# Kernel optimization log

Measured on AMD Instinct MI355X. Metric: run time of the kernel, lower is better.

The kernel has to match this reference:

```python
import jax, jax.numpy as jnp
import numpy as np


def setup_inputs() -> dict:
    key = jax.random.key(0)
    k0, k1, k2, k3, k4 = jax.random.split(key, 5)
    B, H, W, C = 8, 64, 64, 256
    d = C // 8
    scale = 0.02
    return {
        "inputs": jax.random.normal(k0, (B, H, W, C), dtype=jnp.float32),
        "w_q": jax.random.normal(k1, (C, d), dtype=jnp.float32) * scale,
        "w_k": jax.random.normal(k2, (C, d), dtype=jnp.float32) * scale,
        "w_v": jax.random.normal(k3, (C, C), dtype=jnp.float32) * scale,
        "w_out": jax.random.normal(k4, (C, C), dtype=jnp.float32) * scale,
    }


def reference(inputs, w_q, w_k, w_v, w_out):
    B, H, W, C = inputs.shape
    N = H * W
    x = inputs.reshape(B, N, C)  # 1x1 conv == per-pixel channel matmul
    q = jnp.einsum("bnc,cd->bnd", x, w_q)   # [B, N, C//8]
    k = jnp.einsum("bnc,cd->bnd", x, w_k)   # [B, N, C//8]
    v = jnp.einsum("bnc,ce->bne", x, w_v)   # [B, N, C]
    attn = jax.nn.softmax(jnp.einsum("bnd,bmd->bnm", q, k), axis=-1)  # [B, N, N]
    attended = jnp.einsum("bnm,bme->bne", attn, v)  # [B, N, C]
    out = jnp.einsum("bne,ec->bnc", attended, w_out)
    return inputs + out.reshape(B, H, W, C)
```

## Files before the change

kernel.cpp:

```cpp
#include <hip/hip_runtime.h>
#include <hip/hip_bf16.h>
#include <stdint.h>

typedef __attribute__((ext_vector_type(8))) short short8;
typedef __attribute__((ext_vector_type(8))) unsigned short ushort8;
typedef __attribute__((ext_vector_type(4))) unsigned short ushort4v;
typedef __attribute__((ext_vector_type(4))) unsigned u32x4;
typedef __attribute__((ext_vector_type(2))) float f32x2;
typedef __attribute__((ext_vector_type(4))) float f32x4;
typedef __attribute__((ext_vector_type(16))) float f32x16;

#define B_ 8
#define N_ 4096
#define C_ 256
#define D_ 32
#define LOG2E 1.44269504088896f

__device__ inline unsigned short f2bf(float f) {
  union { float f; unsigned u; } v; v.f = f;
  unsigned r = v.u + 0x7fffu + ((v.u >> 16) & 1u);
  return (unsigned short)(r >> 16);
}
__device__ inline float bf2f(unsigned short u) {
  return __uint_as_float(((unsigned)u) << 16);
}
__device__ inline float exp2_fast(float x) {
  float r; asm("v_exp_f32 %0, %1" : "=v"(r) : "v"(x)); return r;
}
__device__ inline unsigned cvt_pk_bf16(float lo, float hi) {
  unsigned r; asm("v_cvt_pk_bf16_f32 %0, %1, %2" : "=v"(r) : "v"(lo), "v"(hi)); return r;
}
__device__ inline void permlane32_swap(unsigned& a, unsigned& b) {
  asm volatile("v_permlane32_swap_b32 %0, %1" : "+v"(a), "+v"(b));
}
__device__ inline void gll16(const unsigned short* src, void* lds) {
  __builtin_amdgcn_global_load_lds((const __attribute__((address_space(1))) void*)src,
                                   (__attribute__((address_space(3))) void*)lds, 16, 0, 0);
}

__device__ inline size_t wf_addr(int C, int kk) {
  int ct = C >> 4, cl = C & 15, s = kk >> 5, gf = (kk >> 3) & 3, j = kk & 7;
  return ((size_t)((ct * 8 + s) * 64 + gf * 16 + cl)) * 8 + j;
}

__global__ __launch_bounds__(256) void prep_kernel(const float* __restrict__ wq,
                                                   const float* __restrict__ wk,
                                                   const float* __restrict__ wo,
                                                   const float* __restrict__ wv,
                                                   unsigned short* __restrict__ wf,
                                                   unsigned short* __restrict__ wv_b,
                                                   unsigned short* __restrict__ woT_b) {
  int i = blockIdx.x * 256 + threadIdx.x;
  if (i < 16384) {
    int C = i >> 8, kk = i & 255;
    float v = (C < 32) ? wq[kk * 32 + C] * LOG2E : wk[kk * 32 + (C - 32)];
    wf[wf_addr(C, kk)] = f2bf(v);
  } else if (i < 81920) {
    int j = i - 16384;
    wv_b[j] = f2bf(wv[j]);
  } else {
    int j = i - 81920;
    int e2 = j >> 8, e = j & 255;
    woT_b[j] = f2bf(wo[e * 256 + e2]);
  }
}

__global__ __launch_bounds__(256) void prep2_kernel(const unsigned short* __restrict__ woT_b,
                                                    const unsigned short* __restrict__ wv_b,
                                                    unsigned short* __restrict__ wf) {
  const int lane = threadIdx.x & 63, w = threadIdx.x >> 6;
  const int g = lane >> 4, li = lane & 15;
  const int m0 = blockIdx.x * 64 + w * 16;
  const unsigned short* arow = woT_b + (size_t)(m0 + li) * 256 + (g << 3);
  const unsigned short* brow = wv_b + (size_t)li * 256 + (g << 3);
  f32x4 acc[16] = {};
  for (int kk = 0; kk < 256; kk += 32) {
    short8 a = *reinterpret_cast<const short8*>(arow + kk);
#pragma unroll
    for (int ct = 0; ct < 16; ++ct) {
      short8 bb = *reinterpret_cast<const short8*>(brow + (size_t)ct * 16 * 256 + kk);
      acc[ct] = __builtin_amdgcn_mfma_f32_16x16x32_bf16(a, bb, acc[ct], 0, 0, 0);
    }
  }
#pragma unroll
  for (int ct = 0; ct < 16; ++ct)
#pragma unroll
    for (int r = 0; r < 4; ++r) {
      const int C = 64 + m0 + (g << 2) + r;
      const int kk = ct * 16 + li;
      wf[wf_addr(C, kk)] = f2bf(acc[ct][r]);
    }
}

__global__ __launch_bounds__(256, 2) void qkv_kernel(const float* __restrict__ x,
                                                     const unsigned short* __restrict__ wf,
                                                     unsigned short* __restrict__ q,
                                                     unsigned short* __restrict__ k,
                                                     unsigned short* __restrict__ vwT) {
  __shared__ __align__(16) unsigned short xs[64 * 256];
  const int tid = threadIdx.x;
  const int l = tid & 63, w = tid >> 6;
  const int bx = blockIdx.x;
  const int g = l >> 4, li = l & 15;
  const int m0 = bx * 64;

  const unsigned short* wfb = wf + (size_t)(w * 5) * 4096;

  short8 BA[5], BB[5];
#pragma unroll
  for (int c = 0; c < 5; ++c)
    BA[c] = *reinterpret_cast<const short8*>(wfb + ((size_t)(c * 8 + 0) * 64 + l) * 8);
#pragma unroll
  for (int c = 0; c < 5; ++c)
    BB[c] = *reinterpret_cast<const short8*>(wfb + ((size_t)(c * 8 + 1) * 64 + l) * 8);

  {
    const int row = tid >> 2, qtr = tid & 3;
    const float* src = x + (size_t)(m0 + row) * 256 + qtr * 64;
    unsigned short* dstrow = xs + row * 256;
#pragma unroll
    for (int jj = 0; jj < 8; ++jj) {
      f32x4 a0 = *reinterpret_cast<const f32x4*>(src + jj * 8);
      f32x4 a1 = *reinterpret_cast<const f32x4*>(src + jj * 8 + 4);
      union { unsigned u[4]; ushort8 v; } P;
      P.u[0] = cvt_pk_bf16(a0[0], a0[1]); P.u[1] = cvt_pk_bf16(a0[2], a0[3]);
      P.u[2] = cvt_pk_bf16(a1[0], a1[1]); P.u[3] = cvt_pk_bf16(a1[2], a1[3]);
      const int blk = (qtr * 8 + jj) ^ (row & 7);
      *reinterpret_cast<ushort8*>(dstrow + blk * 8) = P.v;
    }
  }
  __syncthreads();

  f32x4 acc[4][5] = {};

#define QSTEP(S, BV, WN, PREF)                                                       \
  {                                                                                  \
    asm volatile("s_waitcnt vmcnt(" WN ")" ::: "memory");                            \
    __builtin_amdgcn_sched_barrier(0);                                               \
    short8 a_[4];                                                                    \
    _Pragma("unroll") for (int mt = 0; mt < 4; ++mt) {                               \
      const int row = mt * 16 + li;                                                  \
      a_[mt] = *reinterpret_cast<const short8*>(                                     \
          xs + row * 256 + ((((S) * 4 + g) ^ (row & 7)) << 3));                      \
    }                                                                                \
    _Pragma("unroll") for (int mt = 0; mt < 4; ++mt)                                 \
        _Pragma("unroll") for (int c = 0; c < 5; ++c)                                \
            acc[mt][c] = __builtin_amdgcn_mfma_f32_16x16x32_bf16(a_[mt], BV[c],      \
                                                                 acc[mt][c], 0, 0, 0); \
    if (PREF) {                                                                      \
      _Pragma("unroll") for (int c = 0; c < 5; ++c)                                  \
          BV[c] = *reinterpret_cast<const short8*>(                                  \
              wfb + ((size_t)(c * 8 + (S) + 2) * 64 + l) * 8);                       \
    }                                                                                \
  }

  QSTEP(0, BA, "5", true)
  QSTEP(1, BB, "5", true)
  QSTEP(2, BA, "5", true)
  QSTEP(3, BB, "5", true)
  QSTEP(4, BA, "5", true)
  QSTEP(5, BB, "5", true)
  QSTEP(6, BA, "5", false)
  QSTEP(7, BB, "0", false)
#undef QSTEP

  const int bb_ = bx >> 6;
#pragma unroll
  for (int mt = 0; mt < 4; ++mt) {
    const int nloc = (bx & 63) * 64 + mt * 16 + (g << 2);
#pragma unroll
    for (int c = 0; c < 5; ++c) {
      const int Cg = w * 5 + c;
      if (Cg < 2) {
        const int col = Cg * 16 + li;
#pragma unroll
        for (int r = 0; r < 4; ++r)
          q[((size_t)bb_ * N_ + nloc + r) * D_ + col] = f2bf(acc[mt][c][r]);
      } else if (Cg < 4) {
        const int col = (Cg - 2) * 16 + li;
#pragma unroll
        for (int r = 0; r < 4; ++r)
          k[((size_t)bb_ * N_ + nloc + r) * D_ + col] = f2bf(acc[mt][c][r]);
      } else {
        const int vc = Cg * 16 + li - 64;
        union { unsigned u[2]; ushort4v v; } P;
        P.u[0] = cvt_pk_bf16(acc[mt][c][0], acc[mt][c][1]);
        P.u[1] = cvt_pk_bf16(acc[mt][c][2], acc[mt][c][3]);
        *reinterpret_cast<ushort4v*>(&vwT[((size_t)bb_ * C_ + vc) * N_ + nloc]) = P.v;
      }
    }
  }
}

__global__ __launch_bounds__(512, 2) void flash_kernel(const unsigned short* __restrict__ q,
                                                       const unsigned short* __restrict__ k,
                                                       const unsigned short* __restrict__ vwT,
                                                       const float* __restrict__ x,
                                                       float* __restrict__ out) {
  __shared__ __align__(16) char smem[106496];
  const int tid = threadIdx.x;
  const int l = tid & 63, w_ = tid >> 6;
  const int kvh = w_ >> 2, gw = w_ & 3;
  const int qg = gw >> 1, ch = gw & 1;
  const int blk = blockIdx.x;
  const int b = blk & 7;
  const int qt = blk >> 3;
  const int h = l >> 5, l31 = l & 31;
  const int R = kvh * 53248;

  const unsigned short* kb_ = k + (size_t)b * N_ * D_;
  const unsigned short* vb_ = vwT + (size_t)b * C_ * N_;

  const int qposb = qt * 128 + qg * 64;
  short8 qb[2][2];
#pragma unroll
  for (int qt2 = 0; qt2 < 2; ++qt2) {
    const size_t qoff = ((size_t)b * N_ + qposb + qt2 * 32 + l31) * D_ + h * 8;
    qb[qt2][0] = *reinterpret_cast<const short8*>(q + qoff);
    qb[qt2][1] = *reinterpret_cast<const short8*>(q + qoff + 16);
  }
  asm volatile("s_waitcnt vmcnt(0)" ::: "memory");

  const int stg_row = l >> 2;
  const int stg_bk = ((l & 3) ^ ((l >> 3) & 3)) << 3;
  const int kvbase = kvh * 2048;

#define STAGE_V(BUF, KV0)                                                         \
  {                                                                               \
    char* vd = smem + R + (BUF) * 16384 + gw * 4096;                              \
    _Pragma("unroll") for (int t = 0; t < 4; ++t)                                 \
        gll16(vb_ + (size_t)(gw * 64 + t * 16 + stg_row) * N_ + (KV0) + stg_bk,   \
              vd + t * 1024);                                                     \
  }
#define STAGE_K(BUF, KV0)                                                         \
  {                                                                               \
    if (gw < 2)                                                                   \
      gll16(kb_ + (size_t)((KV0) + gw * 16 + stg_row) * D_ + stg_bk,              \
            smem + R + 49152 + (BUF) * 2048 + gw * 1024);                         \
  }

  f32x16 o[4][2] = {};
  float lsum[2] = {0.f, 0.f};
  const f32x16 z16 = {};

  STAGE_V(0, kvbase)
  STAGE_K(0, kvbase)
  STAGE_V(1, kvbase + 32)

  int cur = 0, nxt = 2;
  for (int i = 0; i < 64; ++i) {
    if (i < 63) { asm volatile("s_waitcnt vmcnt(4)" ::: "memory"); }
    else        { asm volatile("s_waitcnt vmcnt(0)" ::: "memory"); }
    __builtin_amdgcn_sched_barrier(0);
    __builtin_amdgcn_s_barrier();
    if (i < 63) STAGE_K((i + 1) & 1, kvbase + (i + 1) * 32)
    if (i < 62) STAGE_V(nxt, kvbase + (i + 2) * 32)
    const char* Vb = smem + R + cur * 16384;
    const char* Kb = smem + R + 49152 + (i & 1) * 2048;
    const int kkey = (l31 >> 1) & 3;
    short8 ka0 = *reinterpret_cast<const short8*>(Kb + l31 * 64 + (((0 + h) ^ kkey) << 4));
    short8 ka1 = *reinterpret_cast<const short8*>(Kb + l31 * 64 + (((2 + h) ^ kkey) << 4));
    f32x16 s0 = __builtin_amdgcn_mfma_f32_32x32x16_bf16(ka0, qb[0][0], z16, 0, 0, 0);
    s0 = __builtin_amdgcn_mfma_f32_32x32x16_bf16(ka1, qb[0][1], s0, 0, 0, 0);
    f32x16 s1 = __builtin_amdgcn_mfma_f32_32x32x16_bf16(ka0, qb[1][0], z16, 0, 0, 0);
    s1 = __builtin_amdgcn_mfma_f32_32x32x16_bf16(ka1, qb[1][1], s1, 0, 0, 0);
    short8 pf[2][2];
#pragma unroll
    for (int r = 0; r < 16; ++r) s0[r] = exp2_fast(s0[r]);
    if (ch == 0)
      lsum[0] += (((s0[0] + s0[1]) + (s0[2] + s0[3])) + ((s0[4] + s0[5]) + (s0[6] + s0[7]))) +
                 (((s0[8] + s0[9]) + (s0[10] + s0[11])) + ((s0[12] + s0[13]) + (s0[14] + s0[15])));
    {
      unsigned x0 = cvt_pk_bf16(s0[0], s0[1]),   y0 = cvt_pk_bf16(s0[4], s0[5]);
      unsigned x1 = cvt_pk_bf16(s0[2], s0[3]),   y1 = cvt_pk_bf16(s0[6], s0[7]);
      unsigned x2 = cvt_pk_bf16(s0[8], s0[9]),   y2 = cvt_pk_bf16(s0[12], s0[13]);
      unsigned x3 = cvt_pk_bf16(s0[10], s0[11]), y3 = cvt_pk_bf16(s0[14], s0[15]);
      permlane32_swap(x0, y0); permlane32_swap(x1, y1);
      permlane32_swap(x2, y2); permlane32_swap(x3, y3);
      union U { unsigned u[4]; short8 v; };
      U u0; u0.u[0] = x0; u0.u[1] = x1; u0.u[2] = y0; u0.u[3] = y1;
      U u1; u1.u[0] = x2; u1.u[1] = x3; u1.u[2] = y2; u1.u[3] = y3;
      pf[0][0] = u0.v; pf[0][1] = u1.v;
    }
#pragma unroll
    for (int r = 0; r < 16; ++r) s1[r] = exp2_fast(s1[r]);
    if (ch == 0)
      lsum[1] += (((s1[0] + s1[1]) + (s1[2] + s1[3])) + ((s1[4] + s1[5]) + (s1[6] + s1[7]))) +
                 (((s1[8] + s1[9]) + (s1[10] + s1[11])) + ((s1[12] + s1[13]) + (s1[14] + s1[15])));
    {
      unsigned x0 = cvt_pk_bf16(s1[0], s1[1]),   y0 = cvt_pk_bf16(s1[4], s1[5]);
      unsigned x1 = cvt_pk_bf16(s1[2], s1[3]),   y1 = cvt_pk_bf16(s1[6], s1[7]);
      unsigned x2 = cvt_pk_bf16(s1[8], s1[9]),   y2 = cvt_pk_bf16(s1[12], s1[13]);
      unsigned x3 = cvt_pk_bf16(s1[10], s1[11]), y3 = cvt_pk_bf16(s1[14], s1[15]);
      permlane32_swap(x0, y0); permlane32_swap(x1, y1);
      permlane32_swap(x2, y2); permlane32_swap(x3, y3);
      union U { unsigned u[4]; short8 v; };
      U u0; u0.u[0] = x0; u0.u[1] = x1; u0.u[2] = y0; u0.u[3] = y1;
      U u1; u1.u[0] = x2; u1.u[1] = x3; u1.u[2] = y2; u1.u[3] = y3;
      pf[1][0] = u0.v; pf[1][1] = u1.v;
    }
    __builtin_amdgcn_s_setprio(1);
#pragma unroll
    for (int ct = 0; ct < 4; ++ct) {
      const int rl = ch * 128 + ct * 32 + l31;
      const int vkey = (rl >> 1) & 3;
      short8 va0 = *reinterpret_cast<const short8*>(Vb + rl * 64 + (((0 + h) ^ vkey) << 4));
      short8 va1 = *reinterpret_cast<const short8*>(Vb + rl * 64 + (((2 + h) ^ vkey) << 4));
      o[ct][0] = __builtin_amdgcn_mfma_f32_32x32x16_bf16(va0, pf[0][0], o[ct][0], 0, 0, 0);
      o[ct][0] = __builtin_amdgcn_mfma_f32_32x32x16_bf16(va1, pf[0][1], o[ct][0], 0, 0, 0);
      o[ct][1] = __builtin_amdgcn_mfma_f32_32x32x16_bf16(va0, pf[1][0], o[ct][1], 0, 0, 0);
      o[ct][1] = __builtin_amdgcn_mfma_f32_32x32x16_bf16(va1, pf[1][1], o[ct][1], 0, 0, 0);
    }
    __builtin_amdgcn_s_setprio(0);
    cur = (cur == 2) ? 0 : cur + 1;
    nxt = (nxt == 2) ? 0 : nxt + 1;
  }

  lsum[0] += __shfl_xor(lsum[0], 32);
  lsum[1] += __shfl_xor(lsum[1], 32);
  __syncthreads();
  float* lb = reinterpret_cast<float*>(smem + 65536);
  if (ch == 0 && h == 0) {
    lb[kvh * 128 + qg * 64 + l31] = lsum[0];
    lb[kvh * 128 + qg * 64 + 32 + l31] = lsum[1];
  }
  if (kvh == 1) {
    char* ob = smem + gw * 16384;
    int pg = 0;
#pragma unroll
    for (int ct = 0; ct < 4; ++ct)
#pragma unroll
      for (int qt2 = 0; qt2 < 2; ++qt2)
#pragma unroll
        for (int jg = 0; jg < 2; ++jg) {
          u32x4 t;
#pragma unroll
          for (int e = 0; e < 4; ++e) {
            const int j = jg * 4 + e;
            t[e] = cvt_pk_bf16(o[ct][qt2][2 * j], o[ct][qt2][2 * j + 1]);
          }
          *reinterpret_cast<u32x4*>(ob + pg * 1024 + l * 16) = t;
          ++pg;
        }
  }
  __syncthreads();
  if (kvh == 0) {
    float inv[2];
#pragma unroll
    for (int qt2 = 0; qt2 < 2; ++qt2)
      inv[qt2] = 1.0f / (lb[qg * 64 + qt2 * 32 + l31] + lb[128 + qg * 64 + qt2 * 32 + l31]);
    const char* ob = smem + gw * 16384;
    int pg = 0;
#pragma unroll
    for (int ct = 0; ct < 4; ++ct)
#pragma unroll
      for (int qt2 = 0; qt2 < 2; ++qt2)
#pragma unroll
        for (int jg = 0; jg < 2; ++jg) {
          u32x4 t = *reinterpret_cast<const u32x4*>(ob + pg * 1024 + l * 16);
          ++pg;
#pragma unroll
          for (int e = 0; e < 4; ++e) {
            const int j = jg * 4 + e;
            o[ct][qt2][2 * j]     += bf2f((unsigned short)(t[e] & 0xffffu));
            o[ct][qt2][2 * j + 1] += bf2f((unsigned short)(t[e] >> 16));
          }
        }
#pragma unroll
    for (int qt2 = 0; qt2 < 2; ++qt2) {
      const size_t rowbase = ((size_t)b * N_ + qposb + qt2 * 32 + l31) * C_ + ch * 128;
#pragma unroll
      for (int ct = 0; ct < 4; ++ct)
#pragma unroll
        for (int j = 0; j < 8; ++j) {
          const int c = ct * 32 + 2 * (j & 1) + 8 * (j >> 1) + 4 * h;
          f32x2 xr = *reinterpret_cast<const f32x2*>(x + rowbase + c);
          f32x2 t;
          t[0] = o[ct][qt2][2 * j] * inv[qt2] + xr[0];
          t[1] = o[ct][qt2][2 * j + 1] * inv[qt2] + xr[1];
          *reinterpret_cast<f32x2*>(out + rowbase + c) = t;
        }
    }
  }
#undef STAGE_V
#undef STAGE_K
}

extern "C" void kernel_launch(void* const* d_in, const int* in_sizes, int n_in,
                              void* d_out, int out_size, void* d_ws, size_t ws_size,
                              hipStream_t stream) {
  const float* x  = (const float*)d_in[0];
  const float* wq = (const float*)d_in[1];
  const float* wk = (const float*)d_in[2];
  const float* wv = (const float*)d_in[3];
  const float* wo = (const float*)d_in[4];
  float* out = (float*)d_out;
  char* ws = (char*)d_ws;
  unsigned short* wf    = (unsigned short*)(ws + 0);
  unsigned short* wv_b  = (unsigned short*)(ws + 163840);
  unsigned short* woT_b = (unsigned short*)(ws + 294912);
  unsigned short* q     = (unsigned short*)(ws + 425984);
  unsigned short* k     = (unsigned short*)(ws + 2523136);
  unsigned short* vwT   = (unsigned short*)(ws + 4620288);

  prep_kernel<<<576, 256, 0, stream>>>(wq, wk, wo, wv, wf, wv_b, woT_b);
  prep2_kernel<<<4, 256, 0, stream>>>(woT_b, wv_b, wf);
  qkv_kernel<<<512, 256, 0, stream>>>(x, wf, q, k, vwT);
  flash_kernel<<<256, 512, 0, stream>>>(q, k, vwT, x, out);
}
```

Measured before the change: 139.5 us.

## Double KV tile to 64 with double-buffered LDS staging of K and V

Each loop iteration now processes 64 keys instead of 32, so the flash loop runs 32 iterations with half as many block barriers. The old triple-buffered V ring with separate K staging becomes a single double-buffered stage that loads K and V together, using an 8-way XOR swizzle on the wider V rows. The aim is to amortise barrier and wait overhead over more MFMA work per iteration. In exchange LDS grows to 144KB and the wait is now a full vmcnt(0), so prefetch runs only one tile ahead and hides less latency.

```diff
diff --git a/kernel.cpp b/kernel.cpp
--- a/kernel.cpp
+++ b/kernel.cpp
@@ -197,7 +197,7 @@
                                                        const unsigned short* __restrict__ vwT,
                                                        const float* __restrict__ x,
                                                        float* __restrict__ out) {
-  __shared__ __align__(16) char smem[106496];
+  __shared__ __align__(16) char smem[147456];
   const int tid = threadIdx.x;
   const int l = tid & 63, w_ = tid >> 6;
   const int kvh = w_ >> 2, gw = w_ & 3;
@@ -206,7 +206,7 @@
   const int b = blk & 7;
   const int qt = blk >> 3;
   const int h = l >> 5, l31 = l & 31;
-  const int R = kvh * 53248;
+  const int R = kvh * 65536;
 
   const unsigned short* kb_ = k + (size_t)b * N_ * D_;
   const unsigned short* vb_ = vwT + (size_t)b * C_ * N_;
@@ -221,105 +221,102 @@
   }
   asm volatile("s_waitcnt vmcnt(0)" ::: "memory");
 
-  const int stg_row = l >> 2;
-  const int stg_bk = ((l & 3) ^ ((l >> 3) & 3)) << 3;
+  const int vrow = l >> 3;
+  const int vsrc = ((l & 7) ^ ((l >> 3) & 7)) << 3;
+  const int krow = l >> 2;
+  const int ksrc = ((l & 3) ^ ((l >> 3) & 3)) << 3;
   const int kvbase = kvh * 2048;
 
-#define STAGE_V(BUF, KV0)                                                         \
+#define STAGE(BUF, KV0)                                                           \
   {                                                                               \
-    char* vd = smem + R + (BUF) * 16384 + gw * 4096;                              \
-    _Pragma("unroll") for (int t = 0; t < 4; ++t)                                 \
-        gll16(vb_ + (size_t)(gw * 64 + t * 16 + stg_row) * N_ + (KV0) + stg_bk,   \
+    char* vd = smem + R + (BUF) * 32768 + gw * 8192;                              \
+    _Pragma("unroll") for (int t = 0; t < 8; ++t)                                 \
+        gll16(vb_ + (size_t)(gw * 64 + t * 8 + vrow) * N_ + (KV0) + vsrc,         \
               vd + t * 1024);                                                     \
-  }
-#define STAGE_K(BUF, KV0)                                                         \
-  {                                                                               \
-    if (gw < 2)                                                                   \
-      gll16(kb_ + (size_t)((KV0) + gw * 16 + stg_row) * D_ + stg_bk,              \
-            smem + R + 49152 + (BUF) * 2048 + gw * 1024);                         \
+    gll16(kb_ + (size_t)((KV0) + gw * 16 + krow) * D_ + ksrc,                     \
+          smem + 131072 + kvh * 8192 + (BUF) * 4096 + gw * 1024);                 \
   }
 
   f32x16 o[4][2] = {};
   float lsum[2] = {0.f, 0.f};
   const f32x16 z16 = {};
-
-  STAGE_V(0, kvbase)
-  STAGE_K(0, kvbase)
-  STAGE_V(1, kvbase + 32)
-
-  int cur = 0, nxt = 2;
-  for (int i = 0; i < 64; ++i) {
-    if (i < 63) { asm volatile("s_waitcnt vmcnt(4)" ::: "memory"); }
-    else        { asm volatile("s_waitcnt vmcnt(0)" ::: "memory"); }
+  const int kkey = (l31 >> 1) & 3;
+
+  STAGE(0, kvbase)
+
+  for (int i = 0; i < 32; ++i) {
+    const int buf = i & 1;
+    asm volatile("s_waitcnt vmcnt(0)" ::: "memory");
     __builtin_amdgcn_sched_barrier(0);
     __builtin_amdgcn_s_barrier();
-    if (i < 63) STAGE_K((i + 1) & 1, kvbase + (i + 1) * 32)
-    if (i < 62) STAGE_V(nxt, kvbase + (i + 2) * 32)
-    const char* Vb = smem + R + cur * 16384;
-    const char* Kb = smem + R + 49152 + (i & 1) * 2048;
-    const int kkey = (l31 >> 1) & 3;
-    short8 ka0 = *reinterpret_cast<const short8*>(Kb + l31 * 64 + (((0 + h) ^ kkey) << 4));
-    short8 ka1 = *reinterpret_cast<const short8*>(Kb + l31 * 64 + (((2 + h) ^ kkey) << 4));
-    f32x16 s0 = __builtin_amdgcn_mfma_f32_32x32x16_bf16(ka0, qb[0][0], z16, 0, 0, 0);
-    s0 = __builtin_amdgcn_mfma_f32_32x32x16_bf16(ka1, qb[0][1], s0, 0, 0, 0);
-    f32x16 s1 = __builtin_amdgcn_mfma_f32_32x32x16_bf16(ka0, qb[1][0], z16, 0, 0, 0);
-    s1 = __builtin_amdgcn_mfma_f32_32x32x16_bf16(ka1, qb[1][1], s1, 0, 0, 0);
-    short8 pf[2][2];
-#pragma unroll
-    for (int r = 0; r < 16; ++r) s0[r] = exp2_fast(s0[r]);
-    if (ch == 0)
-      lsum[0] += (((s0[0] + s0[1]) + (s0[2] + s0[3])) + ((s0[4] + s0[5]) + (s0[6] + s0[7]))) +
-                 (((s0[8] + s0[9]) + (s0[10] + s0[11])) + ((s0[12] + s0[13]) + (s0[14] + s0[15])));
-    {
-      unsigned x0 = cvt_pk_bf16(s0[0], s0[1]),   y0 = cvt_pk_bf16(s0[4], s0[5]);
-      unsigned x1 = cvt_pk_bf16(s0[2], s0[3]),   y1 = cvt_pk_bf16(s0[6], s0[7]);
-      unsigned x2 = cvt_pk_bf16(s0[8], s0[9]),   y2 = cvt_pk_bf16(s0[12], s0[13]);
-      unsigned x3 = cvt_pk_bf16(s0[10], s0[11]), y3 = cvt_pk_bf16(s0[14], s0[15]);
-      permlane32_swap(x0, y0); permlane32_swap(x1, y1);
-      permlane32_swap(x2, y2); permlane32_swap(x3, y3);
-      union U { unsigned u[4]; short8 v; };
-      U u0; u0.u[0] = x0; u0.u[1] = x1; u0.u[2] = y0; u0.u[3] = y1;
-      U u1; u1.u[0] = x2; u1.u[1] = x3; u1.u[2] = y2; u1.u[3] = y3;
-      pf[0][0] = u0.v; pf[0][1] = u1.v;
-    }
-#pragma unroll
-    for (int r = 0; r < 16; ++r) s1[r] = exp2_fast(s1[r]);
-    if (ch == 0)
-      lsum[1] += (((s1[0] + s1[1]) + (s1[2] + s1[3])) + ((s1[4] + s1[5]) + (s1[6] + s1[7]))) +
-                 (((s1[8] + s1[9]) + (s1[10] + s1[11])) + ((s1[12] + s1[13]) + (s1[14] + s1[15])));
-    {
-      unsigned x0 = cvt_pk_bf16(s1[0], s1[1]),   y0 = cvt_pk_bf16(s1[4], s1[5]);
-      unsigned x1 = cvt_pk_bf16(s1[2], s1[3]),   y1 = cvt_pk_bf16(s1[6], s1[7]);
-      unsigned x2 = cvt_pk_bf16(s1[8], s1[9]),   y2 = cvt_pk_bf16(s1[12], s1[13]);
-      unsigned x3 = cvt_pk_bf16(s1[10], s1[11]), y3 = cvt_pk_bf16(s1[14], s1[15]);
-      permlane32_swap(x0, y0); permlane32_swap(x1, y1);
-      permlane32_swap(x2, y2); permlane32_swap(x3, y3);
-      union U { unsigned u[4]; short8 v; };
-      U u0; u0.u[0] = x0; u0.u[1] = x1; u0.u[2] = y0; u0.u[3] = y1;
-      U u1; u1.u[0] = x2; u1.u[1] = x3; u1.u[2] = y2; u1.u[3] = y3;
-      pf[1][0] = u0.v; pf[1][1] = u1.v;
-    }
-    __builtin_amdgcn_s_setprio(1);
-#pragma unroll
-    for (int ct = 0; ct < 4; ++ct) {
-      const int rl = ch * 128 + ct * 32 + l31;
-      const int vkey = (rl >> 1) & 3;
-      short8 va0 = *reinterpret_cast<const short8*>(Vb + rl * 64 + (((0 + h) ^ vkey) << 4));
-      short8 va1 = *reinterpret_cast<const short8*>(Vb + rl * 64 + (((2 + h) ^ vkey) << 4));
-      o[ct][0] = __builtin_amdgcn_mfma_f32_32x32x16_bf16(va0, pf[0][0], o[ct][0], 0, 0, 0);
-      o[ct][0] = __builtin_amdgcn_mfma_f32_32x32x16_bf16(va1, pf[0][1], o[ct][0], 0, 0, 0);
-      o[ct][1] = __builtin_amdgcn_mfma_f32_32x32x16_bf16(va0, pf[1][0], o[ct][1], 0, 0, 0);
-      o[ct][1] = __builtin_amdgcn_mfma_f32_32x32x16_bf16(va1, pf[1][1], o[ct][1], 0, 0, 0);
-    }
-    __builtin_amdgcn_s_setprio(0);
-    cur = (cur == 2) ? 0 : cur + 1;
-    nxt = (nxt == 2) ? 0 : nxt + 1;
+    if (i < 31) STAGE(buf ^ 1, kvbase + (i + 1) * 64)
+    const char* Vb = smem + R + buf * 32768;
+    const char* Kb = smem + 131072 + kvh * 8192 + buf * 4096;
+#pragma unroll
+    for (int kvt = 0; kvt < 2; ++kvt) {
+      const int krow32 = (kvt * 32 + l31) * 64;
+      short8 ka0 = *reinterpret_cast<const short8*>(Kb + krow32 + (((0 + h) ^ kkey) << 4));
+      short8 ka1 = *reinterpret_cast<const short8*>(Kb + krow32 + (((2 + h) ^ kkey) << 4));
+      f32x16 s0 = __builtin_amdgcn_mfma_f32_32x32x16_bf16(ka0, qb[0][0], z16, 0, 0, 0);
+      s0 = __builtin_amdgcn_mfma_f32_32x32x16_bf16(ka1, qb[0][1], s0, 0, 0, 0);
+      f32x16 s1 = __builtin_amdgcn_mfma_f32_32x32x16_bf16(ka0, qb[1][0], z16, 0, 0, 0);
+      s1 = __builtin_amdgcn_mfma_f32_32x32x16_bf16(ka1, qb[1][1], s1, 0, 0, 0);
+      short8 pf[2][2];
+#pragma unroll
+      for (int r = 0; r < 16; ++r) s0[r] = exp2_fast(s0[r]);
+      if (ch == 0)
+        lsum[0] += (((s0[0] + s0[1]) + (s0[2] + s0[3])) + ((s0[4] + s0[5]) + (s0[6] + s0[7]))) +
+                   (((s0[8] + s0[9]) + (s0[10] + s0[11])) + ((s0[12] + s0[13]) + (s0[14] + s0[15])));
+      {
+        unsigned x0 = cvt_pk_bf16(s0[0], s0[1]),   y0 = cvt_pk_bf16(s0[4], s0[5]);
+        unsigned x1 = cvt_pk_bf16(s0[2], s0[3]),   y1 = cvt_pk_bf16(s0[6], s0[7]);
+        unsigned x2 = cvt_pk_bf16(s0[8], s0[9]),   y2 = cvt_pk_bf16(s0[12], s0[13]);
+        unsigned x3 = cvt_pk_bf16(s0[10], s0[11]), y3 = cvt_pk_bf16(s0[14], s0[15]);
+        permlane32_swap(x0, y0); permlane32_swap(x1, y1);
+        permlane32_swap(x2, y2); permlane32_swap(x3, y3);
+        union U { unsigned u[4]; short8 v; };
+        U u0; u0.u[0] = x0; u0.u[1] = x1; u0.u[2] = y0; u0.u[3] = y1;
+        U u1; u1.u[0] = x2; u1.u[1] = x3; u1.u[2] = y2; u1.u[3] = y3;
+        pf[0][0] = u0.v; pf[0][1] = u1.v;
+      }
+#pragma unroll
+      for (int r = 0; r < 16; ++r) s1[r] = exp2_fast(s1[r]);
+      if (ch == 0)
+        lsum[1] += (((s1[0] + s1[1]) + (s1[2] + s1[3])) + ((s1[4] + s1[5]) + (s1[6] + s1[7]))) +
+                   (((s1[8] + s1[9]) + (s1[10] + s1[11])) + ((s1[12] + s1[13]) + (s1[14] + s1[15])));
+      {
+        unsigned x0 = cvt_pk_bf16(s1[0], s1[1]),   y0 = cvt_pk_bf16(s1[4], s1[5]);
+        unsigned x1 = cvt_pk_bf16(s1[2], s1[3]),   y1 = cvt_pk_bf16(s1[6], s1[7]);
+        unsigned x2 = cvt_pk_bf16(s1[8], s1[9]),   y2 = cvt_pk_bf16(s1[12], s1[13]);
+        unsigned x3 = cvt_pk_bf16(s1[10], s1[11]), y3 = cvt_pk_bf16(s1[14], s1[15]);
+        permlane32_swap(x0, y0); permlane32_swap(x1, y1);
+        permlane32_swap(x2, y2); permlane32_swap(x3, y3);
+        union U { unsigned u[4]; short8 v; };
+        U u0; u0.u[0] = x0; u0.u[1] = x1; u0.u[2] = y0; u0.u[3] = y1;
+        U u1; u1.u[0] = x2; u1.u[1] = x3; u1.u[2] = y2; u1.u[3] = y3;
+        pf[1][0] = u0.v; pf[1][1] = u1.v;
+      }
+      __builtin_amdgcn_s_setprio(1);
+#pragma unroll
+      for (int ct = 0; ct < 4; ++ct) {
+        const int rl = ch * 128 + ct * 32 + l31;
+        const int vkey = rl & 7;
+        const int rb = rl * 128;
+        short8 va0 = *reinterpret_cast<const short8*>(Vb + rb + (((kvt * 4 + 0 + h) ^ vkey) << 4));
+        short8 va1 = *reinterpret_cast<const short8*>(Vb + rb + (((kvt * 4 + 2 + h) ^ vkey) << 4));
+        o[ct][0] = __builtin_amdgcn_mfma_f32_32x32x16_bf16(va0, pf[0][0], o[ct][0], 0, 0, 0);
+        o[ct][0] = __builtin_amdgcn_mfma_f32_32x32x16_bf16(va1, pf[0][1], o[ct][0], 0, 0, 0);
+        o[ct][1] = __builtin_amdgcn_mfma_f32_32x32x16_bf16(va0, pf[1][0], o[ct][1], 0, 0, 0);
+        o[ct][1] = __builtin_amdgcn_mfma_f32_32x32x16_bf16(va1, pf[1][1], o[ct][1], 0, 0, 0);
+      }
+      __builtin_amdgcn_s_setprio(0);
+    }
   }
 
   lsum[0] += __shfl_xor(lsum[0], 32);
   lsum[1] += __shfl_xor(lsum[1], 32);
   __syncthreads();
-  float* lb = reinterpret_cast<float*>(smem + 65536);
+  float* lb = reinterpret_cast<float*>(smem + 131072);
   if (ch == 0 && h == 0) {
     lb[kvh * 128 + qg * 64 + l31] = lsum[0];
     lb[kvh * 128 + qg * 64 + 32 + l31] = lsum[1];
@@ -382,8 +379,7 @@
         }
     }
   }
-#undef STAGE_V
-#undef STAGE_K
+#undef STAGE
 }
 
 extern "C" void kernel_launch(void* const* d_in, const int* in_sizes, int n_in,
```

Measured after the change: 135.7 us. -2.7%, faster.
